# Kernel optimization log

Measured on AMD Instinct MI355X. Metric: run time of the kernel, lower is better.

Reference implementation:

```python
import jax, jax.numpy as jnp
import numpy as np

B, N, C = 8, 4096, 512

def setup_inputs() -> dict:
    key = jax.random.key(0)
    k1, k2, k3, k4, k5, k6 = jax.random.split(key, 6)
    x = jax.random.normal(k1, (B, N, C), dtype=jnp.float32)
    adj = jax.random.uniform(k2, (B, C, C), dtype=jnp.float32)
    # params: stored [in, out] so y = x @ W + b (equivalent to torch Linear)
    s = 1.0 / np.sqrt(C)
    Wqkv = jax.random.uniform(k3, (C, 3 * C), dtype=jnp.float32, minval=-s, maxval=s)
    bqkv = jax.random.uniform(k4, (3 * C,), dtype=jnp.float32, minval=-s, maxval=s)
    Wo = jax.random.uniform(k5, (C, C), dtype=jnp.float32, minval=-s, maxval=s)
    bo = jax.random.uniform(k6, (C,), dtype=jnp.float32, minval=-s, maxval=s)
    return {"x": x, "adj": adj, "Wqkv": Wqkv, "bqkv": bqkv, "Wo": Wo, "bo": bo}

def reference(x, adj, Wqkv, bqkv, Wo, bo):
    # qkv projection + ReLU gating
    qkv = jnp.einsum('bnc,cd->bnd', x, Wqkv) + bqkv          # [B,N,3C]
    q, k, v = jnp.split(qkv, 3, axis=-1)                      # each [B,N,C]
    q, k, v = jax.nn.relu(q), jax.nn.relu(k), jax.nn.relu(v)
    dk = q.shape[-1]
    # channel-wise scores: q^T k over tokens -> [B,C,C]
    scores = jnp.einsum('bnc,bnd->bcd', q, k) / jnp.sqrt(jnp.float32(dk))
    attn = jax.nn.softmax(scores, axis=-1)
    attn = attn * adj                                         # post-softmax adjacency gate
    y = jnp.einsum('bnc,bcd->bnd', v, attn)                   # value.matmul(attention)
    return jnp.einsum('bnc,cd->bnd', y, Wo) + bo
```

## Files before the change

kernel.cpp:

```cpp
#include <hip/hip_runtime.h>

#define B_ 8
#define N_ 4096
#define C_ 512

typedef _Float16 f16;
typedef __attribute__((ext_vector_type(8))) _Float16 f16x8;
typedef __attribute__((ext_vector_type(4))) _Float16 f16x4;
typedef __attribute__((ext_vector_type(4))) float f32x4;

#define TILE_E (128 * 32)

#define GLL16(gsrc, ldst)                                                      \
  __builtin_amdgcn_global_load_lds(                                            \
      (const __attribute__((address_space(1))) void*)(gsrc),                   \
      (__attribute__((address_space(3))) void*)(ldst), 16, 0, 0)

__device__ __forceinline__ int xcd_remap(int bid, int nwg) {
  return (bid & 7) * (nwg >> 3) + (bid >> 3);
}

#define SBAR() asm volatile("s_barrier" ::: "memory")
#define SFENCE() __builtin_amdgcn_sched_barrier(0)

template <int LDA2, int LDB2, int NT>
__device__ __forceinline__ void mainloop8(const char* __restrict__ Agb,
                                          const char* __restrict__ Bgb,
                                          f16* Als, f16* Bls,
                                          f32x4 (&acc)[8][4]) {
  const int tid = threadIdx.x;
  const int lane = tid & 63;
  const int wv = tid >> 6;
  const int wr = wv >> 2;
  const int wcq = wv & 3;

  const int r15 = lane & 15;
  const int kc8 = (lane >> 4) << 3;
  const int swz = (r15 & 7) << 3;
  const int aoff = r15 * 64;
  const int boff = ((wcq & 1) * 64 + r15) * 64;

  int rowl[2], colb[2];
#pragma unroll
  for (int ld = 0; ld < 2; ++ld) {
    const int doff = (ld * 512 + tid) * 16;
    rowl[ld] = doff >> 7;
    colb[ld] = (doff & 127) ^ ((rowl[ld] & 7) << 4);
  }

  auto stage = [&](int t, int mat, int h) {
    if (t >= NT) return;
    const char* gb = mat ? Bgb : Agb;
    const int LD2 = mat ? LDB2 : LDA2;
    f16* lsl = (mat ? Bls : Als) + ((t & 1) * 2 + h) * 8192 + wv * 512;
#pragma unroll
    for (int ld = 0; ld < 2; ++ld)
      GLL16(gb + (size_t)(h * 128 + rowl[ld]) * LD2 + (size_t)t * 128 +
                colb[ld],
            lsl + ld * 4096);
  };

  stage(0, 0, 0); stage(0, 0, 1); stage(0, 1, 0); stage(0, 1, 1);
  stage(1, 0, 0); stage(1, 0, 1); stage(1, 1, 0);
  asm volatile("s_waitcnt vmcnt(6)" ::: "memory");
  SBAR();
  SFENCE();

  for (int T = 0; T < NT; ++T) {
    const f16* Ab = Als + ((T & 1) * 2 + wr) * 8192;
    const f16* Bb = Bls + ((T & 1) * 2 + (wcq >> 1)) * 8192;
    stage(T + 1, 1, 1);
    f16x8 af[8][2], bf[4][2];
#pragma unroll
    for (int m = 0; m < 8; ++m)
#pragma unroll
      for (int s = 0; s < 2; ++s)
        af[m][s] =
            *(const f16x8*)(Ab + aoff + m * 1024 + ((kc8 + s * 32) ^ swz));
    SFENCE();
#pragma unroll
    for (int n = 0; n < 4; ++n)
      bf[n][0] = *(const f16x8*)(Bb + boff + n * 1024 + (kc8 ^ swz));
    SFENCE();
#pragma unroll
    for (int n = 0; n < 4; ++n)
      bf[n][1] = *(const f16x8*)(Bb + boff + n * 1024 + ((kc8 + 32) ^ swz));
    SFENCE();
    SBAR();
    asm volatile("s_waitcnt lgkmcnt(4)" ::: "memory");
    SFENCE();
    __builtin_amdgcn_s_setprio(1);
#pragma unroll
    for (int m = 0; m < 4; ++m)
#pragma unroll
      for (int n = 0; n < 4; ++n)
        acc[m][n] = __builtin_amdgcn_mfma_f32_16x16x32_f16(af[m][0], bf[n][0],
                                                           acc[m][n], 0, 0, 0);
    __builtin_amdgcn_s_setprio(0);
    SBAR();
    SFENCE();
    stage(T + 2, 0, 0);
    SBAR();
    __builtin_amdgcn_s_setprio(1);
#pragma unroll
    for (int m = 4; m < 8; ++m)
#pragma unroll
      for (int n = 0; n < 4; ++n)
        acc[m][n] = __builtin_amdgcn_mfma_f32_16x16x32_f16(af[m][0], bf[n][0],
                                                           acc[m][n], 0, 0, 0);
    __builtin_amdgcn_s_setprio(0);
    SBAR();
    SFENCE();
    stage(T + 2, 0, 1);
    SBAR();
    asm volatile("s_waitcnt lgkmcnt(0)" ::: "memory");
    SFENCE();
    __builtin_amdgcn_s_setprio(1);
#pragma unroll
    for (int m = 0; m < 4; ++m)
#pragma unroll
      for (int n = 0; n < 4; ++n)
        acc[m][n] = __builtin_amdgcn_mfma_f32_16x16x32_f16(af[m][1], bf[n][1],
                                                           acc[m][n], 0, 0, 0);
    __builtin_amdgcn_s_setprio(0);
    SBAR();
    SFENCE();
    stage(T + 2, 1, 0);
    if (T + 2 < NT) {
      asm volatile("s_waitcnt vmcnt(6)" ::: "memory");
    } else {
      asm volatile("s_waitcnt vmcnt(0)" ::: "memory");
    }
    SBAR();
    __builtin_amdgcn_s_setprio(1);
#pragma unroll
    for (int m = 4; m < 8; ++m)
#pragma unroll
      for (int n = 0; n < 4; ++n)
        acc[m][n] = __builtin_amdgcn_mfma_f32_16x16x32_f16(af[m][1], bf[n][1],
                                                           acc[m][n], 0, 0, 0);
    __builtin_amdgcn_s_setprio(0);
    SBAR();
    SFENCE();
  }
}

#define ZERO_ACC8(acc)                                                         \
  f32x4 acc[8][4];                                                             \
  _Pragma("unroll") for (int zi = 0; zi < 8; ++zi)                             \
      _Pragma("unroll") for (int zj = 0; zj < 4; ++zj) {                       \
    f32x4 z = {0.f, 0.f, 0.f, 0.f};                                            \
    acc[zi][zj] = z;                                                           \
  }

__device__ __forceinline__ void run_mainloop(const f16* __restrict__ Atile,
                                             const f16* __restrict__ Btile,
                                             int lda, int ldb, int nk,
                                             f16* As, f16* Bs,
                                             f32x4 (&acc)[4][4]) {
  const int tid = threadIdx.x;
  const int lane = tid & 63;
  const int wave = tid >> 6;
  const int wr = wave >> 1, wc = wave & 1;

  auto stage = [&](int buf, int kt) {
#pragma unroll
    for (int j = 0; j < 2; ++j) {
      const int idx = j * 256 + wave * 64 + lane;
      const int row = idx >> 2;
      const int kc = idx & 3;
      GLL16(Atile + (size_t)row * lda + kt * 32 + kc * 8,
            As + buf * TILE_E + (j * 256 + wave * 64) * 8);
      GLL16(Btile + (size_t)row * ldb + kt * 32 + kc * 8,
            Bs + buf * TILE_E + (j * 256 + wave * 64) * 8);
    }
  };

  stage(0, 0);
  __syncthreads();
  for (int kt = 0; kt < nk; ++kt) {
    const int buf = kt & 1;
    if (kt + 1 < nk) stage(buf ^ 1, kt + 1);
    const f16* aB = As + buf * TILE_E;
    const f16* bB = Bs + buf * TILE_E;
    f16x8 af[4], bf[4];
#pragma unroll
    for (int i = 0; i < 4; ++i)
      af[i] = *(const f16x8*)(aB + (wr * 64 + i * 16 + (lane & 15)) * 32 +
                              ((lane >> 4) * 8));
#pragma unroll
    for (int j = 0; j < 4; ++j)
      bf[j] = *(const f16x8*)(bB + (wc * 64 + j * 16 + (lane & 15)) * 32 +
                              ((lane >> 4) * 8));
#pragma unroll
    for (int i = 0; i < 4; ++i)
#pragma unroll
      for (int j = 0; j < 4; ++j)
        acc[i][j] =
            __builtin_amdgcn_mfma_f32_16x16x32_f16(af[i], bf[j], acc[i][j],
                                                   0, 0, 0);
    __syncthreads();
  }
}

#define ZERO_ACC(acc)                                                          \
  f32x4 acc[4][4];                                                             \
  _Pragma("unroll") for (int zi = 0; zi < 4; ++zi)                             \
      _Pragma("unroll") for (int zj = 0; zj < 4; ++zj) {                       \
    f32x4 z = {0.f, 0.f, 0.f, 0.f};                                            \
    acc[zi][zj] = z;                                                           \
  }

__global__ void __launch_bounds__(256) k_cvt_x(const float* __restrict__ in,
                                               f16* __restrict__ out) {
  const int i = blockIdx.x * 256 + threadIdx.x;
  float4 v = ((const float4*)in)[i];
  f16x4 h = {(f16)v.x, (f16)v.y, (f16)v.z, (f16)v.w};
  ((f16x4*)out)[i] = h;
}

__global__ void __launch_bounds__(256) k_transpose_w(const float* __restrict__ w,
                                                     f16* __restrict__ wt,
                                                     int cols) {
  const int idx = blockIdx.x * 256 + threadIdx.x;
  const int n = idx >> 9;
  const int c = idx & 511;
  wt[idx] = (f16)w[(size_t)c * cols + n];
}

__global__ void __launch_bounds__(512, 2)
    k_gemm_qkv(const f16* __restrict__ x16, const f16* __restrict__ wqkvt,
               const float* __restrict__ bqkv, f16* __restrict__ q_t,
               f16* __restrict__ k_t, f16* __restrict__ v16) {
  __shared__ alignas(16) f16 Als[4 * 8192];
  __shared__ alignas(16) f16 Bls[4 * 8192];
  const int l = xcd_remap(blockIdx.x, 768);
  const int bx = l % 6;
  const int rest = l / 6;
  const int by = rest & 15;
  const int b = rest >> 4;
  const char* Agb = (const char*)(x16 + ((size_t)b * N_ + by * 256) * C_);
  const char* Bgb = (const char*)(wqkvt + (size_t)bx * 256 * C_);
  ZERO_ACC8(acc);
  mainloop8<C_ * 2, C_ * 2, C_ / 64>(Agb, Bgb, Als, Bls, acc);

  const int lane = threadIdx.x & 63, wv = threadIdx.x >> 6;
  const int wr = wv >> 2, wcq = wv & 3;
  const int sec = bx >> 1;
  const int colloc = (bx & 1) * 256 + wcq * 64;
  const int rowbase = by * 256 + wr * 128;
#pragma unroll
  for (int n = 0; n < 4; ++n) {
    const int cch = colloc + n * 16 + (lane & 15);
    const float bias = bqkv[sec * 512 + cch];
#pragma unroll
    for (int m = 0; m < 8; ++m) {
      const int n0 = rowbase + m * 16 + ((lane >> 4) << 2);
      f32x4 a = acc[m][n];
      f16x4 h = {(f16)fmaxf(a[0] + bias, 0.f), (f16)fmaxf(a[1] + bias, 0.f),
                 (f16)fmaxf(a[2] + bias, 0.f), (f16)fmaxf(a[3] + bias, 0.f)};
      if (sec == 0) {
        *(f16x4*)(q_t + ((size_t)b * C_ + cch) * N_ + n0) = h;
      } else if (sec == 1) {
        *(f16x4*)(k_t + ((size_t)b * C_ + cch) * N_ + n0) = h;
      } else {
        f16* dst = v16 + ((size_t)b * N_ + n0) * C_ + cch;
        dst[0] = h[0];
        dst[C_] = h[1];
        dst[2 * C_] = h[2];
        dst[3 * C_] = h[3];
      }
    }
  }
}

__global__ void __launch_bounds__(512, 2)
    k_gemm_scores(const f16* __restrict__ q_t, const f16* __restrict__ k_t,
                  f16* __restrict__ spart) {
  __shared__ alignas(16) f16 Als[4 * 8192];
  __shared__ alignas(16) f16 Bls[4 * 8192];
  const int l = xcd_remap(blockIdx.x, 256);
  const int bx = l & 1;
  const int by = (l >> 1) & 1;
  const int z = l >> 2;
  const int b = z >> 3, sp = z & 7;
  const char* Agb = (const char*)(q_t + (size_t)b * C_ * N_ +
                                  (size_t)(by * 256) * N_ + sp * 512);
  const char* Bgb = (const char*)(k_t + (size_t)b * C_ * N_ +
                                  (size_t)(bx * 256) * N_ + sp * 512);
  ZERO_ACC8(acc);
  mainloop8<N_ * 2, N_ * 2, 8>(Agb, Bgb, Als, Bls, acc);

  const int lane = threadIdx.x & 63, wv = threadIdx.x >> 6;
  const int wr = wv >> 2, wcq = wv & 3;
  f16* base = spart + (size_t)(sp * B_ + b) * C_ * C_;
#pragma unroll
  for (int n = 0; n < 4; ++n) {
    const int d = bx * 256 + wcq * 64 + n * 16 + (lane & 15);
#pragma unroll
    for (int m = 0; m < 8; ++m) {
      const int c0 = by * 256 + wr * 128 + m * 16 + ((lane >> 4) << 2);
#pragma unroll
      for (int r = 0; r < 4; ++r)
        base[(size_t)(c0 + r) * C_ + d] = (f16)acc[m][n][r];
    }
  }
}

__global__ void __launch_bounds__(256)
    k_softmax_gate(const f16* __restrict__ spart,
                   const float* __restrict__ adj, f16* __restrict__ attn) {
  const int b = blockIdx.x >> 9, c = blockIdx.x & 511;
  const int tid = threadIdx.x;
  const size_t ro = ((size_t)b * C_ + c) * C_;
  float s0 = 0.f, s1 = 0.f;
#pragma unroll
  for (int sp = 0; sp < 8; ++sp) {
    const f16* p = spart + (size_t)sp * B_ * C_ * C_ + ro;
    s0 += (float)p[tid];
    s1 += (float)p[tid + 256];
  }
  const float scale = 0.044194173824159216f;
  const float v0 = s0 * scale, v1 = s1 * scale;

  __shared__ float red[256];
  red[tid] = fmaxf(v0, v1);
  __syncthreads();
  for (int s = 128; s > 0; s >>= 1) {
    if (tid < s) red[tid] = fmaxf(red[tid], red[tid + s]);
    __syncthreads();
  }
  const float mx = red[0];
  __syncthreads();
  const float e0 = __expf(v0 - mx), e1 = __expf(v1 - mx);
  red[tid] = e0 + e1;
  __syncthreads();
  for (int s = 128; s > 0; s >>= 1) {
    if (tid < s) red[tid] += red[tid + s];
    __syncthreads();
  }
  const float inv = 1.0f / red[0];
  attn[ro + tid] = (f16)(e0 * inv * adj[ro + tid]);
  attn[ro + tid + 256] = (f16)(e1 * inv * adj[ro + tid + 256]);
}

__global__ void __launch_bounds__(256)
    k_gemm_m(const f16* __restrict__ attn, const f16* __restrict__ wot,
             f16* __restrict__ mt) {
  __shared__ alignas(16) f16 As[2 * TILE_E];
  __shared__ alignas(16) f16 Bs[2 * TILE_E];
  const int b = blockIdx.z;
  const f16* Atile = attn + (size_t)b * C_ * C_ + (size_t)blockIdx.y * 128 * C_;
  const f16* Btile = wot + (size_t)blockIdx.x * 128 * C_;
  ZERO_ACC(acc);
  run_mainloop(Atile, Btile, C_, C_, C_ / 32, As, Bs, acc);

  const int tid = threadIdx.x, lane = tid & 63, wave = tid >> 6;
  const int wr = wave >> 1, wc = wave & 1;
  f16* base = mt + (size_t)b * C_ * C_;
  const int colbase = blockIdx.x * 128 + wc * 64;
  const int rowbase = blockIdx.y * 128 + wr * 64;
#pragma unroll
  for (int j = 0; j < 4; ++j) {
    const int e = colbase + j * 16 + (lane & 15);
#pragma unroll
    for (int i = 0; i < 4; ++i) {
      const int c0 = rowbase + i * 16 + ((lane >> 4) << 2);
      f32x4 a = acc[i][j];
      f16x4 h = {(f16)a[0], (f16)a[1], (f16)a[2], (f16)a[3]};
      *(f16x4*)(base + (size_t)e * C_ + c0) = h;
    }
  }
}

__global__ void __launch_bounds__(512, 2)
    k_gemm_out(const f16* __restrict__ v16, const f16* __restrict__ mt,
               const float* __restrict__ bo, float* __restrict__ out) {
  __shared__ alignas(16) f16 Als[4 * 8192];
  __shared__ alignas(16) f16 Bls[4 * 8192];
  const int l = xcd_remap(blockIdx.x, 256);
  const int bx = l & 1;
  const int by = (l >> 1) & 15;
  const int b = l >> 5;
  const char* Agb = (const char*)(v16 + ((size_t)b * N_ + by * 256) * C_);
  const char* Bgb = (const char*)(mt + (size_t)b * C_ * C_ +
                                  (size_t)(bx * 256) * C_);
  ZERO_ACC8(acc);
  mainloop8<C_ * 2, C_ * 2, 8>(Agb, Bgb, Als, Bls, acc);

  const int lane = threadIdx.x & 63, wv = threadIdx.x >> 6;
  const int wr = wv >> 2, wcq = wv & 3;
  float* base = out + (size_t)b * N_ * C_;
#pragma unroll
  for (int n = 0; n < 4; ++n) {
    const int e = bx * 256 + wcq * 64 + n * 16 + (lane & 15);
    const float bias = bo[e];
#pragma unroll
    for (int m = 0; m < 8; ++m) {
      const int n0 = by * 256 + wr * 128 + m * 16 + ((lane >> 4) << 2);
#pragma unroll
      for (int r = 0; r < 4; ++r)
        base[(size_t)(n0 + r) * C_ + e] = acc[m][n][r] + bias;
    }
  }
}

extern "C" void kernel_launch(void* const* d_in, const int* in_sizes, int n_in,
                              void* d_out, int out_size, void* d_ws,
                              size_t ws_size, hipStream_t stream) {
  const float* x = (const float*)d_in[0];
  const float* adj = (const float*)d_in[1];
  const float* Wqkv = (const float*)d_in[2];
  const float* bqkv = (const float*)d_in[3];
  const float* Wo = (const float*)d_in[4];
  const float* bo = (const float*)d_in[5];
  float* out = (float*)d_out;

  char* ws = (char*)d_ws;
  size_t off = 0;
  auto carve = [&](size_t bytes) -> char* {
    char* p = ws + off;
    off += (bytes + 255) & ~(size_t)255;
    return p;
  };
  f16* x16 = (f16*)carve((size_t)B_ * N_ * C_ * 2);
  f16* wqkvt = (f16*)carve((size_t)3 * C_ * C_ * 2);
  f16* wot = (f16*)carve((size_t)C_ * C_ * 2);
  f16* q_t = (f16*)carve((size_t)B_ * C_ * N_ * 2);
  f16* k_t = (f16*)carve((size_t)B_ * C_ * N_ * 2);
  f16* v16 = (f16*)carve((size_t)B_ * N_ * C_ * 2);
  f16* spart = x16;
  f16* attn16 = k_t;
  f16* mt16 = q_t;

  k_cvt_x<<<(B_ * N_ * C_ / 4) / 256, 256, 0, stream>>>(x, x16);
  k_transpose_w<<<(C_ * 3 * C_) / 256, 256, 0, stream>>>(Wqkv, wqkvt, 3 * C_);
  k_transpose_w<<<(C_ * C_) / 256, 256, 0, stream>>>(Wo, wot, C_);
  k_gemm_qkv<<<768, 512, 0, stream>>>(x16, wqkvt, bqkv, q_t, k_t, v16);
  k_gemm_scores<<<256, 512, 0, stream>>>(q_t, k_t, spart);
  k_softmax_gate<<<B_ * C_, 256, 0, stream>>>(spart, adj, attn16);
  k_gemm_m<<<dim3(4, 4, B_), 256, 0, stream>>>(attn16, wot, mt16);
  k_gemm_out<<<256, 512, 0, stream>>>(v16, mt16, bo, out);
}
```

Baseline: 179.9 us.

## Software-pipeline LDS fragment reads across MFMA groups and restage global loads

Restructures the GEMM mainloop so LDS-to-register fragment reads are split into four groups, each issued ahead of the MFMA group that consumes it. The first group of the next K-tile is prefetched before the last MFMA group of the current tile. Global-to-LDS staging is reordered so the A tiles for T+1 are loaded at the start of each iteration and the B tiles for T+2 near the end, with vmcnt and lgkmcnt waits retuned to match. The goal is to hide LDS read latency and reduce barrier stalls. The cost is tighter buffer-reuse reasoning, with a risk of races if the double-buffer timing is off.

```diff
diff --git a/kernel.cpp b/kernel.cpp
--- a/kernel.cpp
+++ b/kernel.cpp
@@ -22,6 +22,14 @@
 
 #define SBAR() asm volatile("s_barrier" ::: "memory")
 #define SFENCE() __builtin_amdgcn_sched_barrier(0)
+
+#define MFMA_G(MLO, S)                                                         \
+  __builtin_amdgcn_s_setprio(1);                                               \
+  _Pragma("unroll") for (int m = (MLO); m < (MLO) + 4; ++m)                    \
+      _Pragma("unroll") for (int n = 0; n < 4; ++n) acc[m][n] =                \
+          __builtin_amdgcn_mfma_f32_16x16x32_f16(af[m][S], bf[n][S],           \
+                                                 acc[m][n], 0, 0, 0);          \
+  __builtin_amdgcn_s_setprio(0);
 
 template <int LDA2, int LDB2, int NT>
 __device__ __forceinline__ void mainloop8(const char* __restrict__ Agb,
@@ -37,6 +45,8 @@
   const int r15 = lane & 15;
   const int kc8 = (lane >> 4) << 3;
   const int swz = (r15 & 7) << 3;
+  const int k0x = kc8 ^ swz;
+  const int k1x = (kc8 + 32) ^ swz;
   const int aoff = r15 * 64;
   const int boff = ((wcq & 1) * 64 + r15) * 64;
 
@@ -60,86 +70,92 @@
             lsl + ld * 4096);
   };
 
+  f16x8 af[8][2], bf[4][2];
+  auto APTR = [&](int T) -> const f16* {
+    return Als + ((T & 1) * 2 + wr) * 8192;
+  };
+  auto BPTR = [&](int T) -> const f16* {
+    return Bls + ((T & 1) * 2 + (wcq >> 1)) * 8192;
+  };
+  auto rdRG1 = [&](int T) {
+    const f16* Ab = APTR(T);
+    const f16* Bb = BPTR(T);
+#pragma unroll
+    for (int m = 0; m < 4; ++m)
+      af[m][0] = *(const f16x8*)(Ab + aoff + m * 1024 + k0x);
+#pragma unroll
+    for (int n = 0; n < 4; ++n)
+      bf[n][0] = *(const f16x8*)(Bb + boff + n * 1024 + k0x);
+  };
+  auto rdRG2 = [&](int T) {
+    const f16* Ab = APTR(T);
+#pragma unroll
+    for (int m = 4; m < 8; ++m)
+      af[m][0] = *(const f16x8*)(Ab + aoff + m * 1024 + k0x);
+  };
+  auto rdRG3 = [&](int T) {
+    const f16* Ab = APTR(T);
+    const f16* Bb = BPTR(T);
+#pragma unroll
+    for (int m = 0; m < 4; ++m)
+      af[m][1] = *(const f16x8*)(Ab + aoff + m * 1024 + k1x);
+#pragma unroll
+    for (int n = 0; n < 4; ++n)
+      bf[n][1] = *(const f16x8*)(Bb + boff + n * 1024 + k1x);
+  };
+  auto rdRG4 = [&](int T) {
+    const f16* Ab = APTR(T);
+#pragma unroll
+    for (int m = 4; m < 8; ++m)
+      af[m][1] = *(const f16x8*)(Ab + aoff + m * 1024 + k1x);
+  };
+
   stage(0, 0, 0); stage(0, 0, 1); stage(0, 1, 0); stage(0, 1, 1);
-  stage(1, 0, 0); stage(1, 0, 1); stage(1, 1, 0);
-  asm volatile("s_waitcnt vmcnt(6)" ::: "memory");
+  stage(1, 1, 0); stage(1, 1, 1);
+  asm volatile("s_waitcnt vmcnt(4)" ::: "memory");
   SBAR();
   SFENCE();
+  rdRG1(0);
+  SFENCE();
 
   for (int T = 0; T < NT; ++T) {
-    const f16* Ab = Als + ((T & 1) * 2 + wr) * 8192;
-    const f16* Bb = Bls + ((T & 1) * 2 + (wcq >> 1)) * 8192;
-    stage(T + 1, 1, 1);
-    f16x8 af[8][2], bf[4][2];
-#pragma unroll
-    for (int m = 0; m < 8; ++m)
-#pragma unroll
-      for (int s = 0; s < 2; ++s)
-        af[m][s] =
-            *(const f16x8*)(Ab + aoff + m * 1024 + ((kc8 + s * 32) ^ swz));
-    SFENCE();
-#pragma unroll
-    for (int n = 0; n < 4; ++n)
-      bf[n][0] = *(const f16x8*)(Bb + boff + n * 1024 + (kc8 ^ swz));
-    SFENCE();
-#pragma unroll
-    for (int n = 0; n < 4; ++n)
-      bf[n][1] = *(const f16x8*)(Bb + boff + n * 1024 + ((kc8 + 32) ^ swz));
-    SFENCE();
+    stage(T + 1, 0, 0);
+    stage(T + 1, 0, 1);
+    rdRG2(T);
+    asm volatile("s_waitcnt lgkmcnt(4)" ::: "memory");
+    SFENCE();
+    MFMA_G(0, 0);
     SBAR();
+    SFENCE();
+    rdRG3(T);
+    asm volatile("s_waitcnt lgkmcnt(8)" ::: "memory");
+    SFENCE();
+    MFMA_G(4, 0);
+    SBAR();
+    SFENCE();
+    rdRG4(T);
     asm volatile("s_waitcnt lgkmcnt(4)" ::: "memory");
     SFENCE();
-    __builtin_amdgcn_s_setprio(1);
-#pragma unroll
-    for (int m = 0; m < 4; ++m)
-#pragma unroll
-      for (int n = 0; n < 4; ++n)
-        acc[m][n] = __builtin_amdgcn_mfma_f32_16x16x32_f16(af[m][0], bf[n][0],
-                                                           acc[m][n], 0, 0, 0);
-    __builtin_amdgcn_s_setprio(0);
+    MFMA_G(0, 1);
     SBAR();
     SFENCE();
-    stage(T + 2, 0, 0);
-    SBAR();
-    __builtin_amdgcn_s_setprio(1);
-#pragma unroll
-    for (int m = 4; m < 8; ++m)
-#pragma unroll
-      for (int n = 0; n < 4; ++n)
-        acc[m][n] = __builtin_amdgcn_mfma_f32_16x16x32_f16(af[m][0], bf[n][0],
-                                                           acc[m][n], 0, 0, 0);
-    __builtin_amdgcn_s_setprio(0);
-    SBAR();
-    SFENCE();
-    stage(T + 2, 0, 1);
-    SBAR();
-    asm volatile("s_waitcnt lgkmcnt(0)" ::: "memory");
-    SFENCE();
-    __builtin_amdgcn_s_setprio(1);
-#pragma unroll
-    for (int m = 0; m < 4; ++m)
-#pragma unroll
-      for (int n = 0; n < 4; ++n)
-        acc[m][n] = __builtin_amdgcn_mfma_f32_16x16x32_f16(af[m][1], bf[n][1],
-                                                           acc[m][n], 0, 0, 0);
-    __builtin_amdgcn_s_setprio(0);
-    SBAR();
-    SFENCE();
     stage(T + 2, 1, 0);
+    stage(T + 2, 1, 1);
     if (T + 2 < NT) {
-      asm volatile("s_waitcnt vmcnt(6)" ::: "memory");
+      asm volatile("s_waitcnt vmcnt(4)" ::: "memory");
     } else {
       asm volatile("s_waitcnt vmcnt(0)" ::: "memory");
     }
     SBAR();
-    __builtin_amdgcn_s_setprio(1);
-#pragma unroll
-    for (int m = 4; m < 8; ++m)
-#pragma unroll
-      for (int n = 0; n < 4; ++n)
-        acc[m][n] = __builtin_amdgcn_mfma_f32_16x16x32_f16(af[m][1], bf[n][1],
-                                                           acc[m][n], 0, 0, 0);
-    __builtin_amdgcn_s_setprio(0);
+    SFENCE();
+    if (T + 1 < NT) {
+      rdRG1(T + 1);
+      asm volatile("s_waitcnt lgkmcnt(8)" ::: "memory");
+    } else {
+      asm volatile("s_waitcnt lgkmcnt(0)" ::: "memory");
+    }
+    SFENCE();
+    MFMA_G(4, 1);
     SBAR();
     SFENCE();
   }
```

Result: no change. 181.9 us (+1.1%).
